# Kernel tuning notes

Hardware: AMD Instinct MI355X
Metric: run time of the kernel (lower is better)

Reference implementation:

```python
import jax, jax.numpy as jnp
import numpy as np

N = 50000   # nodes
E = 800000  # edges
H = 128     # hidden_dim
H2 = H // 2


def setup_inputs() -> dict:
    key = jax.random.key(0)
    ks = jax.random.split(key, 12)
    s = 0.05  # weight scale for numerical sanity
    d = {}
    d['coord_x'] = jax.random.normal(ks[0], (N,), jnp.float32)
    d['coord_y'] = jax.random.normal(ks[1], (N,), jnp.float32)
    d['W1'] = jax.random.normal(ks[2], (3, H), jnp.float32) * s
    d['b1'] = jnp.zeros((H,), jnp.float32)
    d['W2'] = jax.random.normal(ks[3], (H, H), jnp.float32) * s
    d['b2'] = jnp.zeros((H,), jnp.float32)
    d['W3'] = jax.random.normal(ks[4], (H, H), jnp.float32) * s
    d['b3'] = jnp.zeros((H,), jnp.float32)
    d['W4'] = jax.random.normal(ks[5], (H, H), jnp.float32) * s
    d['b4'] = jnp.zeros((H,), jnp.float32)
    d['W5'] = jax.random.normal(ks[6], (H, H), jnp.float32) * s
    d['b5'] = jnp.zeros((H,), jnp.float32)
    d['Wl1'] = jax.random.normal(ks[7], (H, H2), jnp.float32) * s
    d['bl1'] = jnp.zeros((H2,), jnp.float32)
    d['Wl2'] = jax.random.normal(ks[8], (H2, 1), jnp.float32) * s
    d['bl2'] = jnp.zeros((1,), jnp.float32)
    d['src'] = jax.random.randint(ks[9], (E,), 0, N, dtype=jnp.int32)
    d['dst'] = jax.random.randint(ks[10], (E,), 0, N, dtype=jnp.int32)
    return d


def reference(coord_x, coord_y, W1, b1, W2, b2, W3, b3, W4, b4, W5, b5,
              Wl1, bl1, Wl2, bl2, src, dst):
    ones_e = jnp.ones((E,), jnp.float32)
    in_deg = jax.ops.segment_sum(ones_e, dst, num_segments=N)   # [N]
    out_deg = jax.ops.segment_sum(ones_e, src, num_segments=N)  # [N]
    # DGL GraphConv norm='both': D_out^{-1/2} on src side, D_in^{-1/2} on dst side,
    # degrees clamped to min 1.
    norm_s = (jnp.maximum(out_deg, 1.0) ** -0.5)[:, None]  # [N,1]
    norm_d = (jnp.maximum(in_deg, 1.0) ** -0.5)[:, None]   # [N,1]

    def gconv(h, W, b):
        msg = (h * norm_s)[src]                                   # [E,F] gather
        agg = jax.ops.segment_sum(msg, dst, num_segments=N)       # [N,F] scatter-add
        return (agg * norm_d) @ W + b

    # node features: [in_degree, x, y]
    h = jnp.stack([in_deg, coord_x, coord_y], axis=1)  # [N,3]
    for W, b in ((W1, b1), (W2, b2), (W3, b3), (W4, b4), (W5, b5)):
        h = jax.nn.relu(gconv(h, W, b))

    graph_emb = jnp.mean(h, axis=0, keepdims=True)          # [1,H] mean_nodes
    h_emb = jax.nn.relu(graph_emb @ Wl1 + bl1)              # dropout p=0 -> identity
    pred = jax.nn.sigmoid(h_emb @ Wl2 + bl2)                # [1,1]
    return pred, graph_emb, h
```

## Files before the change

kernel.cpp:

```cpp
#include <hip/hip_runtime.h>
#include <hip/hip_bf16.h>
#include <math.h>

#define NN 50000
#define NE 800000
#define HD 128
#define NB 196
#define CAP 5120
#define B1_EPB 1024

typedef __attribute__((ext_vector_type(8))) short bf16x8v;
typedef __attribute__((ext_vector_type(4))) float f32x4v;

static __device__ __forceinline__ unsigned short f2bf(float x) {
    union { float f; unsigned u; } v; v.f = x;
    unsigned r = v.u + 0x7fff + ((v.u >> 16) & 1);
    return (unsigned short)(r >> 16);
}

__global__ __launch_bounds__(256) void bucket_kernel(const int* __restrict__ src,
                                                     const int* __restrict__ dst,
                                                     int* __restrict__ dcur,
                                                     int* __restrict__ scur,
                                                     int2* __restrict__ dbucket,
                                                     int* __restrict__ sbucket) {
    __shared__ int hd[NB], hsb[NB], cd[NB], cs[NB];
    int t = threadIdx.x;
    if (t < NB) { hd[t] = 0; hsb[t] = 0; }
    __syncthreads();
    int d[4], s[4];
    int e0 = blockIdx.x * B1_EPB + t;
    #pragma unroll
    for (int j = 0; j < 4; ++j) {
        int e = e0 + j * 256;
        if (e < NE) {
            d[j] = dst[e]; s[j] = src[e];
            atomicAdd(&hd[d[j] >> 8], 1);
            atomicAdd(&hsb[s[j] >> 8], 1);
        } else d[j] = -1;
    }
    __syncthreads();
    if (t < NB) {
        cd[t] = atomicAdd(&dcur[t], hd[t]);
        cs[t] = atomicAdd(&scur[t], hsb[t]);
    }
    __syncthreads();
    #pragma unroll
    for (int j = 0; j < 4; ++j) {
        if (d[j] >= 0) {
            int b = d[j] >> 8;
            int p = atomicAdd(&cd[b], 1);
            if (p < CAP) dbucket[(long)b * CAP + p] = make_int2(d[j], s[j]);
            int bs = s[j] >> 8;
            int p2 = atomicAdd(&cs[bs], 1);
            if (p2 < CAP) sbucket[(long)bs * CAP + p2] = s[j];
        }
    }
}

__global__ __launch_bounds__(256) void csr_dst_kernel(const int2* __restrict__ dbucket,
                                                      const int* __restrict__ dcur,
                                                      int* __restrict__ row_ptr,
                                                      int* __restrict__ col) {
    __shared__ int buf[256];
    __shared__ int hist[256];
    __shared__ int cur[256];
    int k = blockIdx.x, t = threadIdx.x;

    int tot = (t < NB) ? min(dcur[t], CAP) : 0;
    buf[t] = tot;
    __syncthreads();
    for (int o = 1; o < 256; o <<= 1) {
        int a = (t >= o) ? buf[t - o] : 0;
        __syncthreads();
        buf[t] += a;
        __syncthreads();
    }
    int base = (k > 0) ? buf[k - 1] : 0;
    int cnt = min(dcur[k], CAP);

    hist[t] = 0;
    __syncthreads();
    const int2* bk = dbucket + (long)k * CAP;
    for (int e = t; e < cnt; e += 256) atomicAdd(&hist[bk[e].x & 255], 1);
    __syncthreads();
    int h = hist[t];

    buf[t] = h;
    __syncthreads();
    for (int o = 1; o < 256; o <<= 1) {
        int a = (t >= o) ? buf[t - o] : 0;
        __syncthreads();
        buf[t] += a;
        __syncthreads();
    }
    int start = base + buf[t] - h;
    int id = (k << 8) + t;
    if (id < NN) row_ptr[id] = start;
    if (k == NB - 1 && t == 0) row_ptr[NN] = base + cnt;
    cur[t] = start;
    __syncthreads();

    for (int e = t; e < cnt; e += 256) {
        int2 p = bk[e];
        int pos = atomicAdd(&cur[p.x & 255], 1);
        col[pos] = p.y;
    }
}

__global__ __launch_bounds__(256) void outdeg_kernel(const int* __restrict__ sbucket,
                                                     const int* __restrict__ scur,
                                                     int* __restrict__ out_cnt) {
    __shared__ int hist[256];
    int k = blockIdx.x, t = threadIdx.x;
    hist[t] = 0;
    __syncthreads();
    int cnt = min(scur[k], CAP);
    const int* bk = sbucket + (long)k * CAP;
    for (int e = t; e < cnt; e += 256) atomicAdd(&hist[bk[e] & 255], 1);
    __syncthreads();
    int id = (k << 8) + t;
    if (id < NN) out_cnt[id] = hist[t];
}

__global__ __launch_bounds__(256) void node_init_kernel(const float* __restrict__ cx,
                                                        const float* __restrict__ cy,
                                                        const int* __restrict__ row_ptr,
                                                        const int* __restrict__ out_cnt,
                                                        float* __restrict__ norm_s,
                                                        float* __restrict__ norm_d,
                                                        float* __restrict__ h0s) {
    int i = blockIdx.x * 256 + threadIdx.x;
    if (i < NN) {
        float id = (float)(row_ptr[i + 1] - row_ptr[i]);
        float od = (float)out_cnt[i];
        float ns = 1.0f / sqrtf(fmaxf(od, 1.0f));
        norm_s[i] = ns;
        norm_d[i] = 1.0f / sqrtf(fmaxf(id, 1.0f));
        h0s[i * 3 + 0] = id * ns;
        h0s[i * 3 + 1] = cx[i] * ns;
        h0s[i * 3 + 2] = cy[i] * ns;
    }
}

__global__ __launch_bounds__(256) void convw_kernel(const float* __restrict__ W2,
                                                    const float* __restrict__ W3,
                                                    const float* __restrict__ W4,
                                                    const float* __restrict__ W5,
                                                    unsigned short* __restrict__ Wt) {
    int gid = blockIdx.x * 256 + threadIdx.x;
    if (gid < 4 * 16384) {
        int l = gid >> 14, idx = gid & 16383;
        int n = idx >> 7, k = idx & 127;
        const float* W = (l == 0) ? W2 : (l == 1) ? W3 : (l == 2) ? W4 : W5;
        Wt[gid] = f2bf(W[k * 128 + n]);
    }
}

__global__ __launch_bounds__(256) void gather3_kernel(const int* __restrict__ row_ptr,
                                                      const int* __restrict__ col,
                                                      const float* __restrict__ h0s,
                                                      const float* __restrict__ norm_d,
                                                      float* __restrict__ agg3) {
    int n = blockIdx.x * 256 + threadIdx.x;
    if (n < NN) {
        float a0 = 0.f, a1 = 0.f, a2 = 0.f;
        int end = row_ptr[n + 1];
        for (int e = row_ptr[n]; e < end; ++e) {
            int s = col[e];
            a0 += h0s[s * 3 + 0];
            a1 += h0s[s * 3 + 1];
            a2 += h0s[s * 3 + 2];
        }
        float nd = norm_d[n];
        agg3[n * 3 + 0] = a0 * nd;
        agg3[n * 3 + 1] = a1 * nd;
        agg3[n * 3 + 2] = a2 * nd;
    }
}

__global__ __launch_bounds__(256) void node3_kernel(const float* __restrict__ agg3,
                                                    const float* __restrict__ norm_s,
                                                    const float* __restrict__ W1,
                                                    const float* __restrict__ b1,
                                                    unsigned short* __restrict__ h1s) {
    int gid = blockIdx.x * 256 + threadIdx.x;
    int i = gid >> 7, c = gid & 127;
    if (i < NN) {
        float a0 = agg3[i * 3 + 0];
        float a1 = agg3[i * 3 + 1];
        float a2 = agg3[i * 3 + 2];
        float v = a0 * W1[c] + a1 * W1[128 + c] + a2 * W1[256 + c] + b1[c];
        h1s[i * 128 + c] = f2bf(fmaxf(v, 0.0f) * norm_s[i]);
    }
}

__global__ __launch_bounds__(256) void gather_bf16_kernel(const int* __restrict__ row_ptr,
                                                          const int* __restrict__ col,
                                                          const unsigned int* __restrict__ hs2,
                                                          const float* __restrict__ norm_d,
                                                          unsigned int* __restrict__ aggb2) {
    int t = threadIdx.x;
    int wave = t >> 6;
    int lane = t & 63;
    int n = blockIdx.x * 4 + wave;
    if (n >= NN) return;
    int beg = row_ptr[n], end = row_ptr[n + 1];
    const unsigned int* hb = hs2 + lane;
    float ax = 0.f, ay = 0.f;
    int e = beg;
    for (; e + 7 < end; e += 8) {
        unsigned u[8];
        #pragma unroll
        for (int j = 0; j < 8; ++j) u[j] = hb[(long)col[e + j] << 6];
        #pragma unroll
        for (int j = 0; j < 8; ++j) {
            ax += __uint_as_float(u[j] << 16);
            ay += __uint_as_float(u[j] & 0xffff0000u);
        }
    }
    for (; e < end; ++e) {
        unsigned u0 = hb[(long)col[e] << 6];
        ax += __uint_as_float(u0 << 16);
        ay += __uint_as_float(u0 & 0xffff0000u);
    }
    float nd = norm_d[n];
    unsigned po = (unsigned)f2bf(ax * nd) | ((unsigned)f2bf(ay * nd) << 16);
    aggb2[(n << 6) + lane] = po;
}

__global__ __launch_bounds__(256) void gemm_mfma_kernel(const unsigned short* __restrict__ aggb,
                                                        const float* __restrict__ scale,
                                                        const unsigned short* __restrict__ Wt,
                                                        const float* __restrict__ bias,
                                                        unsigned short* __restrict__ out_bf,
                                                        float* __restrict__ out_f32,
                                                        float* __restrict__ embsum) {
    __shared__ unsigned short ldsw[128][136];
    __shared__ float ldscol[4][4][128];

    int t = threadIdx.x;
    int wv = t >> 6, lane = t & 63;
    int fr = lane & 15, kq = lane >> 4;
    int m0 = blockIdx.x * 64 + wv * 16;

    #pragma unroll
    for (int i = 0; i < 8; ++i) {
        int idx = t + 256 * i;
        int r = idx >> 4;
        int c8 = (idx & 15) << 3;
        *(bf16x8v*)(&ldsw[r][c8]) = *(const bf16x8v*)(Wt + (r << 7) + c8);
    }

    int mrow = m0 + fr;
    long abase = (long)((mrow < NN) ? mrow : 0) << 7;
    bf16x8v a0 = *(const bf16x8v*)(aggb + abase + 0  + kq * 8);
    bf16x8v a1 = *(const bf16x8v*)(aggb + abase + 32 + kq * 8);
    bf16x8v a2 = *(const bf16x8v*)(aggb + abase + 64 + kq * 8);
    bf16x8v a3 = *(const bf16x8v*)(aggb + abase + 96 + kq * 8);

    float sc[4];
    #pragma unroll
    for (int r = 0; r < 4; ++r) {
        int mr = m0 + kq * 4 + r;
        sc[r] = (out_bf && mr < NN) ? scale[mr] : 1.0f;
    }

    __syncthreads();

    #pragma unroll
    for (int nt = 0; nt < 8; ++nt) {
        int n0 = nt << 4;
        f32x4v acc = {0.f, 0.f, 0.f, 0.f};
        acc = __builtin_amdgcn_mfma_f32_16x16x32_bf16(a0, *(const bf16x8v*)(&ldsw[n0 + fr][0  + kq * 8]), acc, 0, 0, 0);
        acc = __builtin_amdgcn_mfma_f32_16x16x32_bf16(a1, *(const bf16x8v*)(&ldsw[n0 + fr][32 + kq * 8]), acc, 0, 0, 0);
        acc = __builtin_amdgcn_mfma_f32_16x16x32_bf16(a2, *(const bf16x8v*)(&ldsw[n0 + fr][64 + kq * 8]), acc, 0, 0, 0);
        acc = __builtin_amdgcn_mfma_f32_16x16x32_bf16(a3, *(const bf16x8v*)(&ldsw[n0 + fr][96 + kq * 8]), acc, 0, 0, 0);

        float bv = bias[n0 + fr];
        float cs = 0.f;
        #pragma unroll
        for (int r = 0; r < 4; ++r) {
            int mr = m0 + kq * 4 + r;
            if (mr < NN) {
                float v = fmaxf(acc[r] + bv, 0.f);
                if (out_bf) out_bf[((long)mr << 7) + n0 + fr] = f2bf(v * sc[r]);
                else        out_f32[((long)mr << 7) + n0 + fr] = v;
                cs += v;
            }
        }
        if (embsum) ldscol[wv][kq][n0 + fr] = cs;
    }

    if (embsum) {
        __syncthreads();
        if (t < 128) {
            float s = 0.f;
            #pragma unroll
            for (int w = 0; w < 4; ++w)
                #pragma unroll
                for (int q = 0; q < 4; ++q)
                    s += ldscol[w][q][t];
            atomicAdd(&embsum[t], s);
        }
    }
}

__global__ __launch_bounds__(128) void head_kernel(const float* __restrict__ embsum,
                                                   const float* __restrict__ Wl1,
                                                   const float* __restrict__ bl1,
                                                   const float* __restrict__ Wl2,
                                                   const float* __restrict__ bl2,
                                                   float* __restrict__ d_out) {
    __shared__ float emb[128];
    __shared__ float hemb[64];
    int t = threadIdx.x;
    float e = embsum[t] * (1.0f / (float)NN);
    emb[t] = e;
    d_out[1 + t] = e;
    __syncthreads();
    if (t < 64) {
        float acc = bl1[t];
        for (int k = 0; k < 128; ++k)
            acc += emb[k] * Wl1[k * 64 + t];
        hemb[t] = fmaxf(acc, 0.f);
    }
    __syncthreads();
    if (t == 0) {
        float acc = bl2[0];
        for (int j = 0; j < 64; ++j)
            acc += hemb[j] * Wl2[j];
        d_out[0] = 1.0f / (1.0f + expf(-acc));
    }
}

extern "C" void kernel_launch(void* const* d_in, const int* in_sizes, int n_in,
                              void* d_out, int out_size, void* d_ws, size_t ws_size,
                              hipStream_t stream) {
    const float* cx  = (const float*)d_in[0];
    const float* cy  = (const float*)d_in[1];
    const float* W1  = (const float*)d_in[2];
    const float* b1  = (const float*)d_in[3];
    const float* W2  = (const float*)d_in[4];
    const float* b2  = (const float*)d_in[5];
    const float* W3  = (const float*)d_in[6];
    const float* b3  = (const float*)d_in[7];
    const float* W4  = (const float*)d_in[8];
    const float* b4  = (const float*)d_in[9];
    const float* W5  = (const float*)d_in[10];
    const float* b5  = (const float*)d_in[11];
    const float* Wl1 = (const float*)d_in[12];
    const float* bl1 = (const float*)d_in[13];
    const float* Wl2 = (const float*)d_in[14];
    const float* bl2 = (const float*)d_in[15];
    const int*   src = (const int*)d_in[16];
    const int*   dst = (const int*)d_in[17];

    float* out = (float*)d_out;
    float* h_out = out + 129;

    float* ws       = (float*)d_ws;
    float* norm_s   = ws;
    float* norm_d   = ws + NN;
    int*   out_cnt  = (int*)(ws + 2 * NN);
    int*   row_ptr  = (int*)(ws + 3 * NN);
    unsigned short* hs   = (unsigned short*)(ws + 4 * NN + 64);
    unsigned short* aggb = (unsigned short*)(ws + 68 * NN + 64);
    int*   col      = (int*)(ws + 132 * NN + 64);
    float* h0s      = ws + 148 * NN + 64;
    float* agg3     = ws + 151 * NN + 64;
    unsigned short* Wt = (unsigned short*)(ws + 154 * NN + 64);
    float* embsum   = ws + 154 * NN + 64 + 32768;
    int*   dcur     = (int*)(ws + 154 * NN + 33600);
    int*   scur     = dcur + NB;
    int2*  dbucket  = (int2*)(ws + 154 * NN + 34048);
    int*   sbucket  = (int*)(ws + 154 * NN + 34048 + 2 * NB * CAP);

    hipMemsetAsync(dcur, 0, 2 * NB * sizeof(int), stream);
    bucket_kernel<<<(NE + B1_EPB - 1) / B1_EPB, 256, 0, stream>>>(src, dst, dcur, scur,
                                                                  dbucket, sbucket);
    csr_dst_kernel<<<NB, 256, 0, stream>>>(dbucket, dcur, row_ptr, col);
    outdeg_kernel<<<NB, 256, 0, stream>>>(sbucket, scur, out_cnt);

    node_init_kernel<<<(NN + 255) / 256, 256, 0, stream>>>(cx, cy, row_ptr, out_cnt,
                                                           norm_s, norm_d, h0s);
    convw_kernel<<<256, 256, 0, stream>>>(W2, W3, W4, W5, Wt);

    gather3_kernel<<<(NN + 255) / 256, 256, 0, stream>>>(row_ptr, col, h0s, norm_d, agg3);
    node3_kernel<<<(NN * 128) / 256, 256, 0, stream>>>(agg3, norm_s, W1, b1, hs);

    hipMemsetAsync(embsum, 0, 128 * sizeof(float), stream);
    const float* bs[4] = {b2, b3, b4, b5};
    const int gather_blocks = (NN + 3) / 4;
    const int gemm_blocks = (NN + 63) / 64;
    for (int l = 0; l < 4; ++l) {
        gather_bf16_kernel<<<gather_blocks, 256, 0, stream>>>(row_ptr, col,
                                                              (const unsigned int*)hs,
                                                              norm_d,
                                                              (unsigned int*)aggb);
        bool last = (l == 3);
        gemm_mfma_kernel<<<gemm_blocks, 256, 0, stream>>>(
            aggb, norm_s, Wt + l * 16384, bs[l],
            last ? nullptr : hs,
            last ? h_out : nullptr,
            last ? embsum : nullptr);
    }

    head_kernel<<<1, 128, 0, stream>>>(embsum, Wl1, bl1, Wl2, bl2, out);
}
```

Measured before the change: 343.1 us.

## Slice hidden features into 32-column panels and gather per slice

```diff
diff --git a/kernel.cpp b/kernel.cpp
--- a/kernel.cpp
+++ b/kernel.cpp
@@ -17,6 +17,7 @@
     unsigned r = v.u + 0x7fff + ((v.u >> 16) & 1);
     return (unsigned short)(r >> 16);
 }
+
 
 __global__ __launch_bounds__(256) void bucket_kernel(const int* __restrict__ src,
                                                      const int* __restrict__ dst,
@@ -191,42 +192,46 @@
         float a1 = agg3[i * 3 + 1];
         float a2 = agg3[i * 3 + 2];
         float v = a0 * W1[c] + a1 * W1[128 + c] + a2 * W1[256 + c] + b1[c];
-        h1s[i * 128 + c] = f2bf(fmaxf(v, 0.0f) * norm_s[i]);
-    }
-}
-
-__global__ __launch_bounds__(256) void gather_bf16_kernel(const int* __restrict__ row_ptr,
-                                                          const int* __restrict__ col,
-                                                          const unsigned int* __restrict__ hs2,
-                                                          const float* __restrict__ norm_d,
-                                                          unsigned int* __restrict__ aggb2) {
+        h1s[((long)(c >> 5) * NN + i) * 32 + (c & 31)] = f2bf(fmaxf(v, 0.0f) * norm_s[i]);
+    }
+}
+
+__global__ __launch_bounds__(256) void gather_sliced_kernel(const int* __restrict__ row_ptr,
+                                                            const int* __restrict__ col,
+                                                            const unsigned int* __restrict__ hs2,
+                                                            const float* __restrict__ norm_d,
+                                                            unsigned int* __restrict__ aggb2) {
+    int bid = blockIdx.x;
+    int slice = (bid & 7) >> 1;
+    int grp = (bid >> 3) * 2 + (bid & 1);
     int t = threadIdx.x;
-    int wave = t >> 6;
-    int lane = t & 63;
-    int n = blockIdx.x * 4 + wave;
-    if (n >= NN) return;
+    int wave = t >> 6, lane = t & 63;
+    int n = grp * 4 + wave;
+    int sub = lane >> 4, f = lane & 15;
+
     int beg = row_ptr[n], end = row_ptr[n + 1];
-    const unsigned int* hb = hs2 + lane;
+    const unsigned int* hb = hs2 + (long)slice * NN * 16 + f;
     float ax = 0.f, ay = 0.f;
-    int e = beg;
-    for (; e + 7 < end; e += 8) {
-        unsigned u[8];
-        #pragma unroll
-        for (int j = 0; j < 8; ++j) u[j] = hb[(long)col[e + j] << 6];
-        #pragma unroll
-        for (int j = 0; j < 8; ++j) {
-            ax += __uint_as_float(u[j] << 16);
-            ay += __uint_as_float(u[j] & 0xffff0000u);
-        }
-    }
-    for (; e < end; ++e) {
-        unsigned u0 = hb[(long)col[e] << 6];
+    int e = beg + sub;
+    for (; e + 4 < end; e += 8) {
+        int s0 = col[e], s1 = col[e + 4];
+        unsigned u0 = hb[(long)s0 << 4];
+        unsigned u1 = hb[(long)s1 << 4];
+        ax += __uint_as_float(u0 << 16) + __uint_as_float(u1 << 16);
+        ay += __uint_as_float(u0 & 0xffff0000u) + __uint_as_float(u1 & 0xffff0000u);
+    }
+    if (e < end) {
+        unsigned u0 = hb[(long)col[e] << 4];
         ax += __uint_as_float(u0 << 16);
         ay += __uint_as_float(u0 & 0xffff0000u);
     }
-    float nd = norm_d[n];
-    unsigned po = (unsigned)f2bf(ax * nd) | ((unsigned)f2bf(ay * nd) << 16);
-    aggb2[(n << 6) + lane] = po;
+    ax += __shfl_xor(ax, 16); ay += __shfl_xor(ay, 16);
+    ax += __shfl_xor(ax, 32); ay += __shfl_xor(ay, 32);
+    if (sub == 0) {
+        float nd = norm_d[n];
+        unsigned po = (unsigned)f2bf(ax * nd) | ((unsigned)f2bf(ay * nd) << 16);
+        aggb2[((long)slice * NN + n) * 16 + f] = po;
+    }
 }
 
 __global__ __launch_bounds__(256) void gemm_mfma_kernel(const unsigned short* __restrict__ aggb,
@@ -253,11 +258,11 @@
     }
 
     int mrow = m0 + fr;
-    long abase = (long)((mrow < NN) ? mrow : 0) << 7;
-    bf16x8v a0 = *(const bf16x8v*)(aggb + abase + 0  + kq * 8);
-    bf16x8v a1 = *(const bf16x8v*)(aggb + abase + 32 + kq * 8);
-    bf16x8v a2 = *(const bf16x8v*)(aggb + abase + 64 + kq * 8);
-    bf16x8v a3 = *(const bf16x8v*)(aggb + abase + 96 + kq * 8);
+    long mr_ = (mrow < NN) ? mrow : 0;
+    bf16x8v a0 = *(const bf16x8v*)(aggb + (0L * NN + mr_) * 32 + kq * 8);
+    bf16x8v a1 = *(const bf16x8v*)(aggb + (1L * NN + mr_) * 32 + kq * 8);
+    bf16x8v a2 = *(const bf16x8v*)(aggb + (2L * NN + mr_) * 32 + kq * 8);
+    bf16x8v a3 = *(const bf16x8v*)(aggb + (3L * NN + mr_) * 32 + kq * 8);
 
     float sc[4];
     #pragma unroll
@@ -277,19 +282,21 @@
         acc = __builtin_amdgcn_mfma_f32_16x16x32_bf16(a2, *(const bf16x8v*)(&ldsw[n0 + fr][64 + kq * 8]), acc, 0, 0, 0);
         acc = __builtin_amdgcn_mfma_f32_16x16x32_bf16(a3, *(const bf16x8v*)(&ldsw[n0 + fr][96 + kq * 8]), acc, 0, 0, 0);
 
-        float bv = bias[n0 + fr];
+        int c = n0 + fr;
+        long obase = ((long)(c >> 5) * NN) * 32 + (c & 31);
+        float bv = bias[c];
         float cs = 0.f;
         #pragma unroll
         for (int r = 0; r < 4; ++r) {
             int mr = m0 + kq * 4 + r;
             if (mr < NN) {
                 float v = fmaxf(acc[r] + bv, 0.f);
-                if (out_bf) out_bf[((long)mr << 7) + n0 + fr] = f2bf(v * sc[r]);
-                else        out_f32[((long)mr << 7) + n0 + fr] = v;
+                if (out_bf) out_bf[obase + (long)mr * 32] = f2bf(v * sc[r]);
+                else        out_f32[((long)mr << 7) + c] = v;
                 cs += v;
             }
         }
-        if (embsum) ldscol[wv][kq][n0 + fr] = cs;
+        if (embsum) ldscol[wv][kq][c] = cs;
     }
 
     if (embsum) {
@@ -391,13 +398,13 @@
 
     hipMemsetAsync(embsum, 0, 128 * sizeof(float), stream);
     const float* bs[4] = {b2, b3, b4, b5};
-    const int gather_blocks = (NN + 3) / 4;
+    const int gather_blocks = 50000;
     const int gemm_blocks = (NN + 63) / 64;
     for (int l = 0; l < 4; ++l) {
-        gather_bf16_kernel<<<gather_blocks, 256, 0, stream>>>(row_ptr, col,
-                                                              (const unsigned int*)hs,
-                                                              norm_d,
-                                                              (unsigned int*)aggb);
+        gather_sliced_kernel<<<gather_blocks, 256, 0, stream>>>(row_ptr, col,
+                                                                (const unsigned int*)hs,
+                                                                norm_d,
+                                                                (unsigned int*)aggb);
         bool last = (l == 3);
         gemm_mfma_kernel<<<gemm_blocks, 256, 0, stream>>>(
             aggb, norm_s, Wt + l * 16384, bs[l],
```

After: 468.6 us. 36.6% more time.
